# Kernel optimization log

Hardware: AMD Instinct MI355X
Metric: run time of the kernel (lower is better)

The kernel has to match this reference:

```python
import jax, jax.numpy as jnp
import numpy as np

TEMP = 0.3
EPS = 1e-09
EPS2 = 1e-10


def _unit(v):
    return v / jnp.linalg.norm(v, axis=-1, keepdims=True)


def setup_inputs() -> dict:
    key = jax.random.key(0)
    k1, k2 = jax.random.split(key)
    T, Q, D, K = 512, 8, 64, 16  # tracks, queries/track, embed dim, detections/track
    x = _unit(jax.random.normal(k1, (T * K, D), dtype=jnp.float32))
    y = _unit(jax.random.normal(k2, (T, Q, D), dtype=jnp.float32))
    track_idxs = jnp.repeat(jnp.arange(T, dtype=jnp.int64), K)  # every track id present
    return {"x": x, "track_idxs": track_idxs, "y": y}


def reference(x, track_idxs, y):
    # local_contrast=True, separate_tracks=False, static_contrast=False,
    # use_hard_condition=False, shift_to_positive=False (module defaults).
    T, Q, D = y.shape
    # All track ids 0..T-1 appear in track_idxs (by construction), so
    # ut_ids = unique(track_idxs) = arange(T) and y[ut_ids] = y.
    ut_ids = jnp.arange(T, dtype=track_idxs.dtype)
    y_flat = y.reshape(T * Q, D)          # flatten(0,1)
    y_idxs = jnp.tile(ut_ids, Q)          # ut_ids.repeat(Q) in torch semantics
    # Pairwise exp-scaled similarities: [N, T*Q]
    S = jnp.exp(jnp.einsum("nd,md->nm", x, y_flat) / TEMP)
    # Positive pairs: same track id (each x row belongs to exactly one uid),
    # so the per-uid loop collapses to one masked reduction.
    M = track_idxs[:, None] == y_idxs[None, :]
    num = jnp.sum(jnp.where(M, S, 0.0))
    den = jnp.sum(jnp.where(M, 0.0, S))
    loss = -jnp.log(num / (den + num + EPS) + EPS2)
    return loss.reshape(1)
```

## Files before the change

### kernel.cpp

```cpp
#include <hip/hip_runtime.h>
#include <hip/hip_bf16.h>

#define NROWS 8192
#define MROWS 4096
#define DDIM  64
#define TNUM  512
#define BTM   128
#define BTN   128
#define GXM   (NROWS / BTM)
#define GXN   (MROWS / BTN)
#define NBLK_MAIN (GXM * GXN)
#define EXP2_SCALE 4.8089834696298780f

using bf16x8 = __attribute__((ext_vector_type(8))) short;
using f32x4  = __attribute__((ext_vector_type(4))) float;

__device__ __forceinline__ float fast_exp2(float f) {
    return __builtin_amdgcn_exp2f(f);
}
__device__ __forceinline__ short f2bf(float f) {
    __hip_bfloat16 h = __float2bfloat16(f);
    short s; __builtin_memcpy(&s, &h, 2); return s;
}

__device__ __forceinline__ int swz(int row, int colbyte) {
    return ((row << 7) + colbyte) ^ ((row & 7) << 4);
}

extern "C" __global__ __launch_bounds__(256)
void ContrastiveLoss_56435870269983_kernel(
    const float* __restrict__ x, const float* __restrict__ y,
    const int* __restrict__ tid_raw,
    float2* __restrict__ part)
{
    __shared__ short xs[BTM * DDIM];
    __shared__ short ys[BTN * DDIM];
    __shared__ float red[2][256];

    const int t    = threadIdx.x;
    const int lane = t & 63;
    const int wave = t >> 6;
    const int bid  = blockIdx.x;
    const int bx   = bid & (GXM - 1);
    const int by   = bid >> 6;

    const int n0blk = bx * BTM;
    const int m0blk = by * BTN;

    const float4* xsrc = (const float4*)(x + (size_t)n0blk * DDIM);
    const float4* ysrc = (const float4*)(y + (size_t)m0blk * DDIM);
    #pragma unroll
    for (int q = 0; q < 8; ++q) {
        const int g   = q * 256 + t;
        const int row = g >> 4;
        const int c4  = g & 15;
        float4 v = xsrc[g];
        short4 o;
        o.x = f2bf(v.x * EXP2_SCALE); o.y = f2bf(v.y * EXP2_SCALE);
        o.z = f2bf(v.z * EXP2_SCALE); o.w = f2bf(v.w * EXP2_SCALE);
        *(short4*)((char*)xs + swz(row, c4 << 3)) = o;
        float4 w = ysrc[g];
        short4 p;
        p.x = f2bf(w.x); p.y = f2bf(w.y); p.z = f2bf(w.z); p.w = f2bf(w.w);
        *(short4*)((char*)ys + swz(row, c4 << 3)) = p;
    }
    __syncthreads();

    const int n0 = (wave >> 1) * 64;
    const int m0 = (wave & 1) * 64;
    const int rsel = lane & 15;
    const int kb   = (lane >> 4) << 4;

    f32x4 acc[4][4];
    #pragma unroll
    for (int i = 0; i < 4; ++i)
        #pragma unroll
        for (int j = 0; j < 4; ++j) acc[i][j] = (f32x4){0.f, 0.f, 0.f, 0.f};

    #pragma unroll
    for (int s = 0; s < 2; ++s) {
        bf16x8 af[4], bfr[4];
        #pragma unroll
        for (int i = 0; i < 4; ++i)
            af[i] = *(const bf16x8*)((const char*)xs + swz(n0 + i * 16 + rsel, kb + s * 64));
        #pragma unroll
        for (int j = 0; j < 4; ++j)
            bfr[j] = *(const bf16x8*)((const char*)ys + swz(m0 + j * 16 + rsel, kb + s * 64));
        #pragma unroll
        for (int i = 0; i < 4; ++i)
            #pragma unroll
            for (int j = 0; j < 4; ++j)
                acc[i][j] = __builtin_amdgcn_mfma_f32_16x16x32_bf16(
                    af[i], bfr[j], acc[i][j], 0, 0, 0);
    }

    const bool is64 = (tid_raw[17] != 1);
    int tia[4][4];
    #pragma unroll
    for (int i = 0; i < 4; ++i) {
        const int base = n0blk + n0 + i * 16 + (lane >> 4) * 4;
        if (!is64) {
            int4 v = *(const int4*)(tid_raw + base);
            tia[i][0] = v.x; tia[i][1] = v.y; tia[i][2] = v.z; tia[i][3] = v.w;
        } else {
            #pragma unroll
            for (int r = 0; r < 4; ++r) tia[i][r] = tid_raw[2 * (base + r)];
        }
    }
    int yc[4];
    #pragma unroll
    for (int j = 0; j < 4; ++j) yc[j] = (m0blk + m0 + j * 16 + rsel) & (TNUM - 1);

    float sa4[4] = {0.f, 0.f, 0.f, 0.f};
    float sp2[2] = {0.f, 0.f};
    #pragma unroll
    for (int i = 0; i < 4; ++i)
        #pragma unroll
        for (int j = 0; j < 4; ++j)
            #pragma unroll
            for (int r = 0; r < 4; ++r) {
                float e = fast_exp2(acc[i][j][r]);
                sa4[r] += e;
                if (tia[i][r] == yc[j]) sp2[r & 1] += e;
            }
    float sa = (sa4[0] + sa4[1]) + (sa4[2] + sa4[3]);
    float sp = sp2[0] + sp2[1];

    red[0][t] = sa; red[1][t] = sp;
    __syncthreads();
    for (int s = 128; s > 0; s >>= 1) {
        if (t < s) { red[0][t] += red[0][t + s]; red[1][t] += red[1][t + s]; }
        __syncthreads();
    }
    if (t == 0) part[bid] = make_float2(red[0][0], red[1][0]);
}

extern "C" __global__ __launch_bounds__(256)
void cl_final_v9(const float2* __restrict__ part, unsigned int* __restrict__ out)
{
    __shared__ float red[2][256];
    const int t = threadIdx.x;
    float a = 0.0f, p = 0.0f;
    #pragma unroll
    for (int i = t; i < NBLK_MAIN; i += 256) {
        float2 v = part[i];
        a += v.x; p += v.y;
    }
    red[0][t] = a; red[1][t] = p;
    __syncthreads();
    for (int s = 128; s > 0; s >>= 1) {
        if (t < s) { red[0][t] += red[0][t + s]; red[1][t] += red[1][t + s]; }
        __syncthreads();
    }
    if (t == 0) {
        float total = red[0][0];
        float num   = red[1][0];
        float loss  = -__logf(num / (total + 1e-9f) + 1e-10f);
        __hip_bfloat16 bh = __float2bfloat16(loss);
        unsigned short h; __builtin_memcpy(&h, &bh, 2);
        out[0] = ((unsigned int)h << 16) | (unsigned int)h;
    }
}

extern "C" void kernel_launch(void* const* d_in, const int* in_sizes, int n_in,
                              void* d_out, int out_size, void* d_ws, size_t ws_size,
                              hipStream_t stream) {
    const float* x   = (const float*)d_in[0];
    const int*   tid = (const int*)d_in[1];
    const float* y   = (const float*)d_in[2];

    float2* part = (float2*)d_ws;
    ContrastiveLoss_56435870269983_kernel<<<NBLK_MAIN, 256, 0, stream>>>(
        x, y, tid, part);
    cl_final_v9<<<1, 256, 0, stream>>>(part, (unsigned int*)d_out);
}
```

Before: 23.50 us.

## Reuse x tile across two y tiles per block and use wave-shuffle reduction

Each block now handles two 128-row y tiles with one staged x tile. This halves the block count and the x staging work per output, and the next y tile is loaded into shared memory while the exp/mask epilogue of the current one runs. The shared-memory tree reduction is replaced by a per-wave shuffle reduction that writes four partials per block, and the final kernel sums those. The cost is fewer blocks (1024) for parallelism and extra barriers around the y tile reload.

```diff
diff --git a/kernel.cpp b/kernel.cpp
--- a/kernel.cpp
+++ b/kernel.cpp
@@ -7,9 +7,11 @@
 #define TNUM  512
 #define BTM   128
 #define BTN   128
+#define MT    2
 #define GXM   (NROWS / BTM)
-#define GXN   (MROWS / BTN)
-#define NBLK_MAIN (GXM * GXN)
+#define GYM   (MROWS / (BTN * MT))
+#define NBLK_MAIN (GXM * GYM)
+#define NPART (NBLK_MAIN * 4)
 #define EXP2_SCALE 4.8089834696298780f
 
 using bf16x8 = __attribute__((ext_vector_type(8))) short;
@@ -27,6 +29,25 @@
     return ((row << 7) + colbyte) ^ ((row & 7) << 4);
 }
 
+template <bool SCALE>
+__device__ __forceinline__ void stage_tile(const float4* __restrict__ src,
+                                           short* __restrict__ dst, int t) {
+    #pragma unroll
+    for (int q = 0; q < 8; ++q) {
+        const int g = q * 256 + t;
+        const int row = g >> 4, c4 = g & 15;
+        float4 v = src[g];
+        short4 o;
+        if (SCALE) {
+            o.x = f2bf(v.x * EXP2_SCALE); o.y = f2bf(v.y * EXP2_SCALE);
+            o.z = f2bf(v.z * EXP2_SCALE); o.w = f2bf(v.w * EXP2_SCALE);
+        } else {
+            o.x = f2bf(v.x); o.y = f2bf(v.y); o.z = f2bf(v.z); o.w = f2bf(v.w);
+        }
+        *(short4*)((char*)dst + swz(row, c4 << 3)) = o;
+    }
+}
+
 extern "C" __global__ __launch_bounds__(256)
 void ContrastiveLoss_56435870269983_kernel(
     const float* __restrict__ x, const float* __restrict__ y,
@@ -35,64 +56,21 @@
 {
     __shared__ short xs[BTM * DDIM];
     __shared__ short ys[BTN * DDIM];
-    __shared__ float red[2][256];
 
     const int t    = threadIdx.x;
     const int lane = t & 63;
     const int wave = t >> 6;
     const int bid  = blockIdx.x;
     const int bx   = bid & (GXM - 1);
-    const int by   = bid >> 6;
+    const int byg  = bid >> 6;
 
-    const int n0blk = bx * BTM;
-    const int m0blk = by * BTN;
+    const int n0blk  = bx * BTM;
+    const int m0base = byg * (BTN * MT);
 
-    const float4* xsrc = (const float4*)(x + (size_t)n0blk * DDIM);
-    const float4* ysrc = (const float4*)(y + (size_t)m0blk * DDIM);
-    #pragma unroll
-    for (int q = 0; q < 8; ++q) {
-        const int g   = q * 256 + t;
-        const int row = g >> 4;
-        const int c4  = g & 15;
-        float4 v = xsrc[g];
-        short4 o;
-        o.x = f2bf(v.x * EXP2_SCALE); o.y = f2bf(v.y * EXP2_SCALE);
-        o.z = f2bf(v.z * EXP2_SCALE); o.w = f2bf(v.w * EXP2_SCALE);
-        *(short4*)((char*)xs + swz(row, c4 << 3)) = o;
-        float4 w = ysrc[g];
-        short4 p;
-        p.x = f2bf(w.x); p.y = f2bf(w.y); p.z = f2bf(w.z); p.w = f2bf(w.w);
-        *(short4*)((char*)ys + swz(row, c4 << 3)) = p;
-    }
-    __syncthreads();
-
-    const int n0 = (wave >> 1) * 64;
-    const int m0 = (wave & 1) * 64;
+    const int n0   = (wave >> 1) * 64;
+    const int m0w  = (wave & 1) * 64;
     const int rsel = lane & 15;
     const int kb   = (lane >> 4) << 4;
-
-    f32x4 acc[4][4];
-    #pragma unroll
-    for (int i = 0; i < 4; ++i)
-        #pragma unroll
-        for (int j = 0; j < 4; ++j) acc[i][j] = (f32x4){0.f, 0.f, 0.f, 0.f};
-
-    #pragma unroll
-    for (int s = 0; s < 2; ++s) {
-        bf16x8 af[4], bfr[4];
-        #pragma unroll
-        for (int i = 0; i < 4; ++i)
-            af[i] = *(const bf16x8*)((const char*)xs + swz(n0 + i * 16 + rsel, kb + s * 64));
-        #pragma unroll
-        for (int j = 0; j < 4; ++j)
-            bfr[j] = *(const bf16x8*)((const char*)ys + swz(m0 + j * 16 + rsel, kb + s * 64));
-        #pragma unroll
-        for (int i = 0; i < 4; ++i)
-            #pragma unroll
-            for (int j = 0; j < 4; ++j)
-                acc[i][j] = __builtin_amdgcn_mfma_f32_16x16x32_bf16(
-                    af[i], bfr[j], acc[i][j], 0, 0, 0);
-    }
 
     const bool is64 = (tid_raw[17] != 1);
     int tia[4][4];
@@ -107,42 +85,80 @@
             for (int r = 0; r < 4; ++r) tia[i][r] = tid_raw[2 * (base + r)];
         }
     }
-    int yc[4];
-    #pragma unroll
-    for (int j = 0; j < 4; ++j) yc[j] = (m0blk + m0 + j * 16 + rsel) & (TNUM - 1);
+
+    stage_tile<true >((const float4*)(x + (size_t)n0blk * DDIM), xs, t);
+    stage_tile<false>((const float4*)(y + (size_t)m0base * DDIM), ys, t);
+    __syncthreads();
 
     float sa4[4] = {0.f, 0.f, 0.f, 0.f};
     float sp2[2] = {0.f, 0.f};
+
     #pragma unroll
-    for (int i = 0; i < 4; ++i)
+    for (int mt = 0; mt < MT; ++mt) {
+        f32x4 acc[4][4];
         #pragma unroll
-        for (int j = 0; j < 4; ++j)
+        for (int i = 0; i < 4; ++i)
             #pragma unroll
-            for (int r = 0; r < 4; ++r) {
-                float e = fast_exp2(acc[i][j][r]);
-                sa4[r] += e;
-                if (tia[i][r] == yc[j]) sp2[r & 1] += e;
-            }
+            for (int j = 0; j < 4; ++j) acc[i][j] = (f32x4){0.f, 0.f, 0.f, 0.f};
+
+        #pragma unroll
+        for (int s = 0; s < 2; ++s) {
+            bf16x8 af[4], bfr[4];
+            #pragma unroll
+            for (int i = 0; i < 4; ++i)
+                af[i] = *(const bf16x8*)((const char*)xs + swz(n0 + i * 16 + rsel, kb + s * 64));
+            #pragma unroll
+            for (int j = 0; j < 4; ++j)
+                bfr[j] = *(const bf16x8*)((const char*)ys + swz(m0w + j * 16 + rsel, kb + s * 64));
+            #pragma unroll
+            for (int i = 0; i < 4; ++i)
+                #pragma unroll
+                for (int j = 0; j < 4; ++j)
+                    acc[i][j] = __builtin_amdgcn_mfma_f32_16x16x32_bf16(
+                        af[i], bfr[j], acc[i][j], 0, 0, 0);
+        }
+        __syncthreads();
+
+        if (mt + 1 < MT)
+            stage_tile<false>((const float4*)(y + (size_t)(m0base + (mt + 1) * BTN) * DDIM), ys, t);
+
+        const int mrow = m0base + mt * BTN + m0w;
+        int yc[4];
+        #pragma unroll
+        for (int j = 0; j < 4; ++j) yc[j] = (mrow + j * 16 + rsel) & (TNUM - 1);
+        #pragma unroll
+        for (int i = 0; i < 4; ++i)
+            #pragma unroll
+            for (int j = 0; j < 4; ++j)
+                #pragma unroll
+                for (int r = 0; r < 4; ++r) {
+                    float e = fast_exp2(acc[i][j][r]);
+                    sa4[r] += e;
+                    if (tia[i][r] == yc[j]) sp2[r & 1] += e;
+                }
+
+        if (mt + 1 < MT) __syncthreads();
+    }
+
     float sa = (sa4[0] + sa4[1]) + (sa4[2] + sa4[3]);
     float sp = sp2[0] + sp2[1];
 
-    red[0][t] = sa; red[1][t] = sp;
-    __syncthreads();
-    for (int s = 128; s > 0; s >>= 1) {
-        if (t < s) { red[0][t] += red[0][t + s]; red[1][t] += red[1][t + s]; }
-        __syncthreads();
+    #pragma unroll
+    for (int off = 32; off; off >>= 1) {
+        sa += __shfl_down(sa, off, 64);
+        sp += __shfl_down(sp, off, 64);
     }
-    if (t == 0) part[bid] = make_float2(red[0][0], red[1][0]);
+    if (lane == 0) part[bid * 4 + wave] = make_float2(sa, sp);
 }
 
 extern "C" __global__ __launch_bounds__(256)
-void cl_final_v9(const float2* __restrict__ part, unsigned int* __restrict__ out)
+void cl_final_v10(const float2* __restrict__ part, unsigned int* __restrict__ out)
 {
     __shared__ float red[2][256];
     const int t = threadIdx.x;
     float a = 0.0f, p = 0.0f;
     #pragma unroll
-    for (int i = t; i < NBLK_MAIN; i += 256) {
+    for (int i = t; i < NPART; i += 256) {
         float2 v = part[i];
         a += v.x; p += v.y;
     }
@@ -172,5 +188,5 @@
     float2* part = (float2*)d_ws;
     ContrastiveLoss_56435870269983_kernel<<<NBLK_MAIN, 256, 0, stream>>>(
         x, y, tid, part);
-    cl_final_v9<<<1, 256, 0, stream>>>(part, (unsigned int*)d_out);
+    cl_final_v10<<<1, 256, 0, stream>>>(part, (unsigned int*)d_out);
 }
```

New measurement: 22.21 us. 5.5% less time.
